# Performance work log

Hardware: AMD Instinct MI355X
Metric: run time of the kernel (lower is better)

Reference implementation:

```python
import jax, jax.numpy as jnp
import numpy as np

# Model dims
B, T, D = 1, 2048, 2048          # batch, seq_len, d_model
HI, DI = 4, 64                   # indexer heads / dim
H, DH = 16, 128                  # attention heads / head dim (H*DH == D)
TOPK = 512                       # sparse top-k tokens per query
NEG = -1e9


def setup_inputs() -> dict:
    key = jax.random.key(0)
    ks = jax.random.split(key, 8)
    s = 0.02  # weight init scale
    return {
        "hidden_states": jax.random.normal(ks[0], (B, T, D), jnp.float32),
        "Wq_idx": jax.random.normal(ks[1], (D, HI * DI), jnp.float32) * s,
        "Wk_idx": jax.random.normal(ks[2], (D, DI), jnp.float32) * s,
        "Ww_idx": jax.random.normal(ks[3], (D, HI), jnp.float32) * s,
        "Wq": jax.random.normal(ks[4], (D, H * DH), jnp.float32) * s,
        "Wk": jax.random.normal(ks[5], (D, H * DH), jnp.float32) * s,
        "Wv": jax.random.normal(ks[6], (D, H * DH), jnp.float32) * s,
        "Wo": jax.random.normal(ks[7], (H * DH, D), jnp.float32) * s,
    }


def reference(hidden_states, Wq_idx, Wk_idx, Ww_idx, Wq, Wk, Wv, Wo):
    x = hidden_states
    # ---- Lightning indexer: I[t,s] = sum_j w[t,j] * relu(q[t,j] . k[s]) ----
    qi = (x @ Wq_idx).reshape(B, T, HI, DI)          # [B,T,HI,DI]
    ki = x @ Wk_idx                                   # [B,S,DI]
    w = x @ Ww_idx                                    # [B,T,HI]
    dots = jnp.einsum('bthd,bsd->bths', qi, ki)       # [B,T,HI,S]
    index_scores = (jax.nn.relu(dots) * w[..., None]).sum(axis=2)  # [B,T,S]

    # ---- Top-k token selection with causal mask ----
    causal = jnp.triu(jnp.ones((T, T), dtype=bool), 1)            # True above diag
    masked_scores = jnp.where(causal[None], NEG, index_scores)
    _, top_idx = jax.lax.top_k(masked_scores, TOPK)               # [B,T,TOPK]
    b_ix = jnp.arange(B)[:, None, None]
    t_ix = jnp.arange(T)[None, :, None]
    top_mask = jnp.zeros((B, T, T), dtype=bool).at[b_ix, t_ix, top_idx].set(True)
    add_mask = jnp.where(top_mask, 0.0, NEG).astype(x.dtype)      # [B,T,S]

    # ---- Dense multi-head attention with additive sparse mask ----
    q = (x @ Wq).reshape(B, T, H, DH)
    k = (x @ Wk).reshape(B, T, H, DH)
    v = (x @ Wv).reshape(B, T, H, DH)
    scores = jnp.einsum('bthd,bshd->bhts', q, k) / np.sqrt(DH).astype(np.float32)
    scores = scores + add_mask[:, None]                            # [B,H,T,S]
    probs = jax.nn.softmax(scores, axis=-1)
    attn = jnp.einsum('bhts,bshd->bthd', probs, v).reshape(B, T, H * DH)
    attn_output = attn @ Wo                                        # [B,T,D]
    return attn_output
```

## Files before the change

kernel.cpp:

```cpp
#include <hip/hip_runtime.h>
#include <cstdint>
#include <cstddef>

#define T_DIM 2048
#define D_DIM 2048
#define HI_N 4
#define DI_N 64
#define H_N 16
#define DH_N 128
#define TOPK_N 512
#define NEG_F (-1e9f)
#define FA_NEG (-1e30f)

typedef __attribute__((ext_vector_type(8))) short short8;
typedef __attribute__((ext_vector_type(4))) float f32x4;
typedef unsigned short ushort_t;

__device__ __forceinline__ unsigned short f2bf(float f) {
  unsigned u = __float_as_uint(f);
  u += 0x7FFFu + ((u >> 16) & 1u);
  return (unsigned short)(u >> 16);
}
__device__ __forceinline__ float bf2f(unsigned short b) {
  return __uint_as_float((unsigned)b << 16);
}

__global__ __launch_bounds__(256) void idx_proj(const float* __restrict__ x,
                                                const float* __restrict__ Wq_idx,
                                                const float* __restrict__ Wk_idx,
                                                const float* __restrict__ Ww_idx,
                                                float* __restrict__ qi,
                                                float* __restrict__ ki,
                                                float* __restrict__ wI) {
  __shared__ float As[2][16][64];
  __shared__ float Bs[2][16][64];
  const int bm = blockIdx.y << 6;
  const int bn_id = blockIdx.x;
  const float* B; float* C; int ldB, cb, ncols;
  if (bn_id < 4)       { B = Wq_idx; C = qi; ldB = 256; cb = bn_id << 6; ncols = 64; }
  else if (bn_id == 4) { B = Wk_idx; C = ki; ldB = 64;  cb = 0;          ncols = 64; }
  else                 { B = Ww_idx; C = wI; ldB = 4;   cb = 0;          ncols = 4;  }
  const int tid = threadIdx.x;
  const int tx = tid & 15, ty = tid >> 4;
  const int am = tid >> 2;
  const int ak = (tid & 3) << 2;
  float acc[4][4] = {};

  float4 a4 = *(const float4*)&x[(size_t)(bm + am) * 2048 + ak];
  float4 b4 = make_float4(0, 0, 0, 0);
  if ((tx << 2) < ncols) b4 = *(const float4*)&B[(size_t)ty * ldB + cb + (tx << 2)];
  As[0][ak + 0][am] = a4.x; As[0][ak + 1][am] = a4.y;
  As[0][ak + 2][am] = a4.z; As[0][ak + 3][am] = a4.w;
  *(float4*)&Bs[0][ty][tx << 2] = b4;

  int p = 0;
  for (int k0 = 0; k0 < 2048; k0 += 16) {
    __syncthreads();
    const bool more = (k0 + 16) < 2048;
    if (more) {
      a4 = *(const float4*)&x[(size_t)(bm + am) * 2048 + k0 + 16 + ak];
      if ((tx << 2) < ncols)
        b4 = *(const float4*)&B[(size_t)(k0 + 16 + ty) * ldB + cb + (tx << 2)];
    }
#pragma unroll
    for (int kk = 0; kk < 16; ++kk) {
      float4 av4 = *(const float4*)&As[p][kk][ty << 2];
      float4 bv4 = *(const float4*)&Bs[p][kk][tx << 2];
      float av[4] = {av4.x, av4.y, av4.z, av4.w};
      float bv[4] = {bv4.x, bv4.y, bv4.z, bv4.w};
#pragma unroll
      for (int i = 0; i < 4; ++i)
#pragma unroll
        for (int j = 0; j < 4; ++j) acc[i][j] += av[i] * bv[j];
    }
    if (more) {
      As[1 - p][ak + 0][am] = a4.x; As[1 - p][ak + 1][am] = a4.y;
      As[1 - p][ak + 2][am] = a4.z; As[1 - p][ak + 3][am] = a4.w;
      *(float4*)&Bs[1 - p][ty][tx << 2] = b4;
    }
    p ^= 1;
  }
#pragma unroll
  for (int i = 0; i < 4; ++i) {
    int m = bm + (ty << 2) + i;
    int n0 = tx << 2;
    if (n0 + 3 < ncols) {
      *(float4*)&C[(size_t)m * ldB + cb + n0] =
          make_float4(acc[i][0], acc[i][1], acc[i][2], acc[i][3]);
    } else {
#pragma unroll
      for (int j = 0; j < 4; ++j)
        if (n0 + j < ncols) C[(size_t)m * ldB + cb + n0 + j] = acc[i][j];
    }
  }
}

__global__ __launch_bounds__(256) void cast_bf16(const float* __restrict__ in,
                                                 ushort_t* __restrict__ out) {
  int i = (blockIdx.x * 256 + threadIdx.x) * 4;
  float4 f = *(const float4*)(in + i);
  ushort4 o;
  o.x = f2bf(f.x); o.y = f2bf(f.y); o.z = f2bf(f.z); o.w = f2bf(f.w);
  *(ushort4*)(out + i) = o;
}

__global__ __launch_bounds__(256) void cast_transpose(const float* __restrict__ in,
                                                      ushort_t* __restrict__ out,
                                                      int R, int C) {
  __shared__ float tile[32][33];
  const int bx = blockIdx.x * 32;
  const int by = blockIdx.y * 32;
  const int tx = threadIdx.x & 31, ty = threadIdx.x >> 5;
#pragma unroll
  for (int i = 0; i < 32; i += 8)
    tile[ty + i][tx] = in[(size_t)(by + ty + i) * C + bx + tx];
  __syncthreads();
#pragma unroll
  for (int i = 0; i < 32; i += 8)
    out[(size_t)(bx + ty + i) * R + by + tx] = f2bf(tile[tx][ty + i]);
}

__global__ __launch_bounds__(256) void transpose_bf(const ushort_t* __restrict__ in,
                                                    ushort_t* __restrict__ out,
                                                    int ldin) {
  __shared__ ushort_t tile[64][68];
  const int bx = blockIdx.x * 64;
  const int by = blockIdx.y * 64;
  const int tid = threadIdx.x;
#pragma unroll
  for (int p = 0; p < 4; ++p) {
    int r = p * 16 + (tid >> 4), c0 = (tid & 15) * 4;
    *(ushort4*)&tile[r][c0] = *(const ushort4*)(in + (size_t)(by + r) * ldin + bx + c0);
  }
  __syncthreads();
#pragma unroll
  for (int p = 0; p < 4; ++p) {
    int r = p * 16 + (tid >> 4), c0 = (tid & 15) * 4;
    ushort4 o;
    o.x = tile[c0 + 0][r]; o.y = tile[c0 + 1][r];
    o.z = tile[c0 + 2][r]; o.w = tile[c0 + 3][r];
    *(ushort4*)(out + (size_t)(bx + r) * T_DIM + by + c0) = o;
  }
}

template <int OUT_BF16>
__global__ __launch_bounds__(256) void gemm_bt(const ushort_t* __restrict__ A,
                                               const ushort_t* __restrict__ Bt,
                                               void* __restrict__ C,
                                               int M, int N, int K) {
  __shared__ __attribute__((aligned(16))) ushort_t As[128 * 64];
  __shared__ __attribute__((aligned(16))) ushort_t Bs[128 * 64];
  const int bm = blockIdx.y << 7;
  const int bn = blockIdx.x << 7;
  const int tid = threadIdx.x;
  const int lane = tid & 63;
  const int wv = tid >> 6;
  const int wm = (wv >> 1) << 6;
  const int wn = (wv & 1) << 6;

  f32x4 acc[4][4] = {};

  const int sr = tid >> 3;
  const int sc = (tid & 7) << 3;
  const ushort_t* ga = A + (size_t)(bm + sr) * K + sc;
  const ushort_t* gb = Bt + (size_t)(bn + sr) * K + sc;
  const size_t rstep = (size_t)32 * K;

  for (int k0 = 0; k0 < K; k0 += 64) {
#pragma unroll
    for (int i = 0; i < 4; ++i) {
      __builtin_amdgcn_global_load_lds(
          (const __attribute__((address_space(1))) unsigned int*)(ga + i * rstep + k0),
          (__attribute__((address_space(3))) unsigned int*)(As + i * 2048 + tid * 8),
          16, 0, 0);
      __builtin_amdgcn_global_load_lds(
          (const __attribute__((address_space(1))) unsigned int*)(gb + i * rstep + k0),
          (__attribute__((address_space(3))) unsigned int*)(Bs + i * 2048 + tid * 8),
          16, 0, 0);
    }
    __syncthreads();
#pragma unroll
    for (int ks = 0; ks < 2; ++ks) {
      short8 af[4], bfr[4];
      const int kk = (ks << 5) + ((lane >> 4) << 3);
#pragma unroll
      for (int i = 0; i < 4; ++i) {
        af[i]  = *(const short8*)(As + (wm + (i << 4) + (lane & 15)) * 64 + kk);
        bfr[i] = *(const short8*)(Bs + (wn + (i << 4) + (lane & 15)) * 64 + kk);
      }
#pragma unroll
      for (int i = 0; i < 4; ++i)
#pragma unroll
        for (int j = 0; j < 4; ++j)
          acc[i][j] = __builtin_amdgcn_mfma_f32_16x16x32_bf16(af[i], bfr[j], acc[i][j], 0, 0, 0);
    }
    __syncthreads();
  }

  const int lrow = (lane >> 4) << 2;
  const int lcol = lane & 15;
#pragma unroll
  for (int i = 0; i < 4; ++i) {
    const int row = bm + wm + (i << 4) + lrow;
#pragma unroll
    for (int j = 0; j < 4; ++j) {
      const int col = bn + wn + (j << 4) + lcol;
#pragma unroll
      for (int r = 0; r < 4; ++r) {
        if (OUT_BF16)
          ((ushort_t*)C)[(size_t)(row + r) * N + col] = f2bf(acc[i][j][r]);
        else
          ((float*)C)[(size_t)(row + r) * N + col] = acc[i][j][r];
      }
    }
  }
}

__global__ __launch_bounds__(256) void idx_scores_rt(const float* __restrict__ qi,
                                                     const float* __restrict__ ki,
                                                     const float* __restrict__ w,
                                                     float* __restrict__ out) {
  const int t0 = blockIdx.y << 6, s0 = blockIdx.x << 6;
  const int tid = threadIdx.x;
  const int tx = tid & 15, ty = tid >> 4;
  if (s0 > t0 + 63) {
    const float4 nf = make_float4(NEG_F, NEG_F, NEG_F, NEG_F);
#pragma unroll
    for (int i = 0; i < 4; ++i) {
      int m = t0 + (ty << 2) + i;
      *(float4*)&out[(size_t)m * T_DIM + s0 + (tx << 2)] = nf;
    }
    return;
  }
  __shared__ float As[16][64];
  __shared__ float Bs[16][64];
  __shared__ float wsh[64][4];
  if (tid < 64) *(float4*)wsh[tid] = *(const float4*)&w[(size_t)(t0 + tid) * 4];
  const int am = tid >> 2;
  const int ak = (tid & 3) << 2;
  float oacc[4][4] = {};
#pragma unroll
  for (int h = 0; h < HI_N; ++h) {
    float dacc[4][4] = {};
    for (int k0 = 0; k0 < DI_N; k0 += 16) {
      float4 qa = *(const float4*)&qi[(size_t)(t0 + am) * 256 + h * DI_N + k0 + ak];
      float4 kb = *(const float4*)&ki[(size_t)(s0 + am) * DI_N + k0 + ak];
      __syncthreads();
      As[ak + 0][am] = qa.x; As[ak + 1][am] = qa.y;
      As[ak + 2][am] = qa.z; As[ak + 3][am] = qa.w;
      Bs[ak + 0][am] = kb.x; Bs[ak + 1][am] = kb.y;
      Bs[ak + 2][am] = kb.z; Bs[ak + 3][am] = kb.w;
      __syncthreads();
#pragma unroll
      for (int kk = 0; kk < 16; ++kk) {
        float4 a4 = *(const float4*)&As[kk][ty << 2];
        float4 b4 = *(const float4*)&Bs[kk][tx << 2];
        float av[4] = {a4.x, a4.y, a4.z, a4.w};
        float bv[4] = {b4.x, b4.y, b4.z, b4.w};
#pragma unroll
        for (int i = 0; i < 4; ++i)
#pragma unroll
          for (int j = 0; j < 4; ++j) dacc[i][j] += av[i] * bv[j];
      }
    }
#pragma unroll
    for (int i = 0; i < 4; ++i) {
      float wh = wsh[(ty << 2) + i][h];
#pragma unroll
      for (int j = 0; j < 4; ++j) oacc[i][j] += fmaxf(dacc[i][j], 0.f) * wh;
    }
  }
#pragma unroll
  for (int i = 0; i < 4; ++i) {
    int m = t0 + (ty << 2) + i;
    int n0 = s0 + (tx << 2);
    float4 r;
    r.x = (n0 + 0 > m) ? NEG_F : oacc[i][0];
    r.y = (n0 + 1 > m) ? NEG_F : oacc[i][1];
    r.z = (n0 + 2 > m) ? NEG_F : oacc[i][2];
    r.w = (n0 + 3 > m) ? NEG_F : oacc[i][3];
    *(float4*)&out[(size_t)m * T_DIM + n0] = r;
  }
}

__global__ __launch_bounds__(256) void select_mask(const float* __restrict__ scores,
                                                   unsigned long long* __restrict__ maskbits) {
  const int t = blockIdx.x, tid = threadIdx.x;
  __shared__ unsigned int hist[256];
  __shared__ unsigned int s_prefix, s_krem;
  __shared__ unsigned char bytes[256];
  unsigned int uv[8];
  const float* row = scores + (size_t)t * T_DIM;
  {
    float4 f0 = *(const float4*)(row + tid * 8);
    float4 f1 = *(const float4*)(row + tid * 8 + 4);
    float fv[8] = {f0.x, f0.y, f0.z, f0.w, f1.x, f1.y, f1.z, f1.w};
#pragma unroll
    for (int j = 0; j < 8; ++j) {
      unsigned u = __float_as_uint(fv[j]);
      uv[j] = (u & 0x80000000u) ? ~u : (u | 0x80000000u);
    }
  }
  if (tid == 0) { s_prefix = 0u; s_krem = TOPK_N; }
  for (int p = 0; p < 4; ++p) {
    const int sh = 24 - 8 * p;
    hist[tid] = 0;
    __syncthreads();
    const unsigned pm = p ? (0xFFFFFFFFu << (32 - 8 * p)) : 0u;
    const unsigned prefix = s_prefix;
#pragma unroll
    for (int j = 0; j < 8; ++j)
      if ((uv[j] & pm) == prefix) atomicAdd(&hist[(uv[j] >> sh) & 255], 1u);
    __syncthreads();
    if (tid == 0) {
      unsigned krem = s_krem, cum = 0;
      int b = 255;
      for (;; --b) { cum += hist[b]; if (cum >= krem) break; }
      s_prefix = prefix | ((unsigned)b << sh);
      s_krem = krem - (cum - hist[b]);
    }
    __syncthreads();
  }
  const unsigned V = s_prefix;
  const int kr = (int)s_krem;
  int eqc = 0;
#pragma unroll
  for (int j = 0; j < 8; ++j) eqc += (uv[j] == V);
  __syncthreads();
  hist[tid] = (unsigned)eqc;
  __syncthreads();
  for (int off = 1; off < 256; off <<= 1) {
    int v = (int)hist[tid];
    if (tid >= off) v += (int)hist[tid - off];
    __syncthreads();
    hist[tid] = (unsigned)v;
    __syncthreads();
  }
  int run = (int)hist[tid] - eqc;
  unsigned char byte = 0;
#pragma unroll
  for (int j = 0; j < 8; ++j) {
    bool eq = (uv[j] == V);
    bool take = (uv[j] > V) || (eq && run < kr);
    run += eq;
    byte |= (unsigned char)(take ? (1u << j) : 0u);
  }
  bytes[tid] = byte;
  __syncthreads();
  if (tid < 32) {
    unsigned long long wqw = 0;
#pragma unroll
    for (int b = 0; b < 8; ++b)
      wqw |= (unsigned long long)bytes[tid * 8 + b] << (8 * b);
    maskbits[(size_t)t * 32 + tid] = wqw;
  }
}

__global__ __launch_bounds__(256, 1) void flash_attn(
    const ushort_t* __restrict__ q, const ushort_t* __restrict__ k,
    const ushort_t* __restrict__ vt, const unsigned long long* __restrict__ maskbits,
    ushort_t* __restrict__ attn, int ldqk) {
  __shared__ __attribute__((aligned(16))) ushort_t Ks[128 * 128];
  __shared__ __attribute__((aligned(16))) ushort_t Vts[128 * 128];
  __shared__ __attribute__((aligned(16))) ushort_t Ps[128 * 136];
  __shared__ float mstate[2][128], lstate[2][128];
  __shared__ float pmax[2][128], psum[2][128];

  const int tt = blockIdx.x;
  const int h  = blockIdx.y;
  const int t0 = tt << 7;
  const int tid = threadIdx.x;
  const int lane = tid & 63;
  const int wv = tid >> 6;
  const int wm = (wv >> 1) << 6;
  const int wn = (wv & 1) << 6;
  const int l15 = lane & 15, l4 = lane >> 4;

  {
    const ushort_t* gq = q + (size_t)(t0 + (tid >> 4)) * ldqk + h * DH_N + (tid & 15) * 8;
#pragma unroll
    for (int p = 0; p < 8; ++p)
      __builtin_amdgcn_global_load_lds(
          (const __attribute__((address_space(1))) unsigned int*)(gq + (size_t)p * 16 * ldqk),
          (__attribute__((address_space(3))) unsigned int*)(Ks + p * 2048 + tid * 8), 16, 0, 0);
  }
  __syncthreads();
  short8 qfrag[4][4];
#pragma unroll
  for (int ks = 0; ks < 4; ++ks)
#pragma unroll
    for (int i = 0; i < 4; ++i)
      qfrag[ks][i] = *(const short8*)(Ks + (wm + i * 16 + l15) * 128 + ks * 32 + l4 * 8);
  if (tid < 128) { mstate[0][tid] = -INFINITY; lstate[0][tid] = 0.f; }

  f32x4 acc[4][4] = {};
  const int nst = (tt < 4) ? 4 : (tt + 1);
  const bool owner = ((wv & 1) == 0) && (l15 == 0);
  const float rsc = 0.08838834764831845f;

  for (int st = 0; st < nst; ++st) {
    const int s0 = st << 7;
    __syncthreads();
    {
      const ushort_t* gk = k + (size_t)(s0 + (tid >> 4)) * ldqk + h * DH_N + (tid & 15) * 8;
      const ushort_t* gv = vt + (size_t)(h * DH_N + (tid >> 4)) * T_DIM + s0 + (tid & 15) * 8;
#pragma unroll
      for (int p = 0; p < 8; ++p) {
        __builtin_amdgcn_global_load_lds(
            (const __attribute__((address_space(1))) unsigned int*)(gk + (size_t)p * 16 * ldqk),
            (__attribute__((address_space(3))) unsigned int*)(Ks + p * 2048 + tid * 8), 16, 0, 0);
        __builtin_amdgcn_global_load_lds(
            (const __attribute__((address_space(1))) unsigned int*)(gv + (size_t)p * 16 * T_DIM),
            (__attribute__((address_space(3))) unsigned int*)(Vts + p * 2048 + tid * 8), 16, 0, 0);
      }
    }
    unsigned long long mw[4][4];
    {
      const int wbase = (s0 >> 6) + (wn >> 6);
#pragma unroll
      for (int i = 0; i < 4; ++i)
#pragma unroll
        for (int r = 0; r < 4; ++r)
          mw[i][r] = maskbits[(size_t)(t0 + wm + i * 16 + l4 * 4 + r) * 32 + wbase];
    }
    __syncthreads();

    f32x4 sacc[4][4] = {};
#pragma unroll
    for (int ks = 0; ks < 4; ++ks) {
      short8 bfr[4];
#pragma unroll
      for (int j = 0; j < 4; ++j)
        bfr[j] = *(const short8*)(Ks + (wn + j * 16 + l15) * 128 + ks * 32 + l4 * 8);
#pragma unroll
      for (int i = 0; i < 4; ++i)
#pragma unroll
        for (int j = 0; j < 4; ++j)
          sacc[i][j] = __builtin_amdgcn_mfma_f32_16x16x32_bf16(qfrag[ks][i], bfr[j], sacc[i][j], 0, 0, 0);
    }
#pragma unroll
    for (int i = 0; i < 4; ++i)
#pragma unroll
      for (int j = 0; j < 4; ++j)
#pragma unroll
        for (int r = 0; r < 4; ++r) {
          bool sel = (mw[i][r] >> (j * 16 + l15)) & 1;
          sacc[i][j][r] = sel ? sacc[i][j][r] * rsc : FA_NEG;
        }
    float pmx[4][4];
#pragma unroll
    for (int i = 0; i < 4; ++i)
#pragma unroll
      for (int r = 0; r < 4; ++r) {
        float m0 = fmaxf(fmaxf(sacc[i][0][r], sacc[i][1][r]), fmaxf(sacc[i][2][r], sacc[i][3][r]));
#pragma unroll
        for (int off = 1; off < 16; off <<= 1) m0 = fmaxf(m0, __shfl_xor(m0, off));
        pmx[i][r] = m0;
      }
    if (l15 == 0)
#pragma unroll
      for (int i = 0; i < 4; ++i)
#pragma unroll
        for (int r = 0; r < 4; ++r)
          pmax[wv & 1][wm + i * 16 + l4 * 4 + r] = pmx[i][r];
    __syncthreads();

    const int rp = st & 1, wp = 1 - rp;
    float nmr[4][4];
#pragma unroll
    for (int i = 0; i < 4; ++i)
#pragma unroll
      for (int r = 0; r < 4; ++r) {
        int rw = wm + i * 16 + l4 * 4 + r;
        nmr[i][r] = fmaxf(mstate[rp][rw], fmaxf(pmax[0][rw], pmax[1][rw]));
      }
    float alpha_c[4];
#pragma unroll
    for (int j = 0; j < 4; ++j) {
      int col = wn + j * 16 + l15;
      float mo = mstate[rp][col];
      float nc = fmaxf(mo, fmaxf(pmax[0][col], pmax[1][col]));
      alpha_c[j] = __expf(mo - nc);
    }
    if (owner)
#pragma unroll
      for (int i = 0; i < 4; ++i)
#pragma unroll
        for (int r = 0; r < 4; ++r)
          mstate[wp][wm + i * 16 + l4 * 4 + r] = nmr[i][r];

    float psr[4][4] = {};
#pragma unroll
    for (int i = 0; i < 4; ++i)
#pragma unroll
      for (int j = 0; j < 4; ++j)
#pragma unroll
        for (int r = 0; r < 4; ++r) {
          float s = sacc[i][j][r];
          float pv = (s <= -1e29f) ? 0.f : __expf(s - nmr[i][r]);
          sacc[i][j][r] = pv;
          psr[i][r] += pv;
        }
#pragma unroll
    for (int i = 0; i < 4; ++i)
#pragma unroll
      for (int j = 0; j < 4; ++j) {
        int col = wn + j * 16 + l15;
#pragma unroll
        for (int r = 0; r < 4; ++r)
          Ps[(wm + i * 16 + l4 * 4 + r) * 136 + col] = f2bf(sacc[i][j][r]);
      }
#pragma unroll
    for (int i = 0; i < 4; ++i)
#pragma unroll
      for (int r = 0; r < 4; ++r) {
        float sv = psr[i][r];
#pragma unroll
        for (int off = 1; off < 16; off <<= 1) sv += __shfl_xor(sv, off);
        psr[i][r] = sv;
      }
    if (l15 == 0)
#pragma unroll
      for (int i = 0; i < 4; ++i)
#pragma unroll
        for (int r = 0; r < 4; ++r)
          psum[wv & 1][wm + i * 16 + l4 * 4 + r] = psr[i][r];
#pragma unroll
    for (int i = 0; i < 4; ++i)
#pragma unroll
      for (int j = 0; j < 4; ++j)
#pragma unroll
        for (int r = 0; r < 4; ++r)
          acc[i][j][r] *= alpha_c[j];
    __syncthreads();

    if (owner)
#pragma unroll
      for (int i = 0; i < 4; ++i)
#pragma unroll
        for (int r = 0; r < 4; ++r) {
          int rw = wm + i * 16 + l4 * 4 + r;
          float al = __expf(mstate[rp][rw] - nmr[i][r]);
          lstate[wp][rw] = al * lstate[rp][rw] + psum[0][rw] + psum[1][rw];
        }
#pragma unroll
    for (int ks = 0; ks < 4; ++ks) {
      short8 af[4], bfr[4];
#pragma unroll
      for (int i = 0; i < 4; ++i)
        af[i] = *(const short8*)(Vts + (wm + i * 16 + l15) * 128 + ks * 32 + l4 * 8);
#pragma unroll
      for (int j = 0; j < 4; ++j)
        bfr[j] = *(const short8*)(Ps + (wn + j * 16 + l15) * 136 + ks * 32 + l4 * 8);
#pragma unroll
      for (int i = 0; i < 4; ++i)
#pragma unroll
        for (int j = 0; j < 4; ++j)
          acc[i][j] = __builtin_amdgcn_mfma_f32_16x16x32_bf16(af[i], bfr[j], acc[i][j], 0, 0, 0);
    }
  }
  __syncthreads();
  const int fp = nst & 1;
  float linv[4];
#pragma unroll
  for (int j = 0; j < 4; ++j) linv[j] = 1.f / lstate[fp][wn + j * 16 + l15];
#pragma unroll
  for (int i = 0; i < 4; ++i)
#pragma unroll
    for (int j = 0; j < 4; ++j) {
      int col = wn + j * 16 + l15;
      int dbase = wm + i * 16 + l4 * 4;
      ushort4 pk;
      pk.x = f2bf(acc[i][j][0] * linv[j]);
      pk.y = f2bf(acc[i][j][1] * linv[j]);
      pk.z = f2bf(acc[i][j][2] * linv[j]);
      pk.w = f2bf(acc[i][j][3] * linv[j]);
      *(ushort4*)(Ps + col * 136 + dbase) = pk;
    }
  __syncthreads();
#pragma unroll
  for (int p = 0; p < 8; ++p) {
    int rw = p * 16 + (tid >> 4);
    int d0 = (tid & 15) * 8;
    *(ulonglong2*)(attn + (size_t)(t0 + rw) * D_DIM + h * DH_N + d0) =
        *(const ulonglong2*)(Ps + rw * 136 + d0);
  }
}

extern "C" void kernel_launch(void* const* d_in, const int* in_sizes, int n_in,
                              void* d_out, int out_size, void* d_ws, size_t ws_size,
                              hipStream_t stream) {
  (void)in_sizes; (void)n_in; (void)out_size; (void)ws_size;
  const float* x      = (const float*)d_in[0];
  const float* Wq_idx = (const float*)d_in[1];
  const float* Wk_idx = (const float*)d_in[2];
  const float* Ww_idx = (const float*)d_in[3];
  const float* Wq     = (const float*)d_in[4];
  const float* Wk     = (const float*)d_in[5];
  const float* Wv     = (const float*)d_in[6];
  const float* Wo     = (const float*)d_in[7];
  float* out = (float*)d_out;

  char* ws = (char*)d_ws;
  const size_t MB = 1ull << 20;
  float*    scores  = (float*)(ws);
  ushort_t* qkv_bf  = (ushort_t*)(ws);
  unsigned long long* maskbits = (unsigned long long*)(ws + 25 * MB + 512 * 1024);
  ushort_t* x_bf    = (ushort_t*)(ws + 26 * MB);
  ushort_t* Wcat_t  = (ushort_t*)(ws + 34 * MB);
  ushort_t* vt_bf   = (ushort_t*)(ws + 34 * MB);
  ushort_t* attn_bf = (ushort_t*)(ws + 42 * MB);
  ushort_t* Wo_t    = (ushort_t*)(ws + 58 * MB);
  float*    qi      = (float*)(ws + 66 * MB);
  float*    ki      = (float*)(ws + 68 * MB);
  float*    wI      = (float*)(ws + 68 * MB + 512 * 1024);

  const dim3 blk(256);
  const dim3 tgrid(D_DIM / 32, D_DIM / 32);

  cast_bf16<<<dim3((D_DIM * T_DIM) / 1024), blk, 0, stream>>>(x, x_bf);
  cast_transpose<<<tgrid, blk, 0, stream>>>(Wq, Wcat_t, D_DIM, D_DIM);
  cast_transpose<<<tgrid, blk, 0, stream>>>(Wk, Wcat_t + (size_t)D_DIM * D_DIM, D_DIM, D_DIM);
  cast_transpose<<<tgrid, blk, 0, stream>>>(Wv, Wcat_t + (size_t)2 * D_DIM * D_DIM, D_DIM, D_DIM);
  cast_transpose<<<tgrid, blk, 0, stream>>>(Wo, Wo_t, D_DIM, D_DIM);

  idx_proj<<<dim3(6, T_DIM / 64), blk, 0, stream>>>(x, Wq_idx, Wk_idx, Ww_idx, qi, ki, wI);
  idx_scores_rt<<<dim3(T_DIM / 64, T_DIM / 64), blk, 0, stream>>>(qi, ki, wI, scores);
  select_mask<<<dim3(T_DIM), blk, 0, stream>>>(scores, maskbits);

  gemm_bt<1><<<dim3(3 * D_DIM / 128, T_DIM / 128), blk, 0, stream>>>(
      x_bf, Wcat_t, qkv_bf, T_DIM, 3 * D_DIM, D_DIM);

  transpose_bf<<<dim3(D_DIM / 64, T_DIM / 64), blk, 0, stream>>>(
      qkv_bf + 2 * D_DIM, vt_bf, 3 * D_DIM);

  flash_attn<<<dim3(T_DIM / 128, H_N), blk, 0, stream>>>(
      qkv_bf, qkv_bf + D_DIM, vt_bf, maskbits, attn_bf, 3 * D_DIM);

  gemm_bt<0><<<dim3(D_DIM / 128, T_DIM / 128), blk, 0, stream>>>(
      attn_bf, Wo_t, out, T_DIM, D_DIM, D_DIM);
}
```

Measured before the change: 597.8 us.

## Double-buffer K tiles with prefetch, XOR-swizzle LDS, and fine-grained waitcnt barriers in flash attention

Makes the K tile double-buffered in shared memory so the next tile's K load is issued during the current iteration. Replaces __syncthreads with explicit vmcnt/lgkmcnt waits plus s_barrier so V loads can still be in flight while QK^T and softmax run. Adds an XOR swizzle to the Q/K/V LDS layout to cut bank conflicts on fragment reads, and raises wave priority around the MFMA loops. This costs an extra 32 KB of LDS, and the hand-counted vmcnt values must exactly match the outstanding loads or the kernel reads stale data.

```diff
diff --git a/kernel.cpp b/kernel.cpp
--- a/kernel.cpp
+++ b/kernel.cpp
@@ -360,7 +360,7 @@
     const ushort_t* __restrict__ q, const ushort_t* __restrict__ k,
     const ushort_t* __restrict__ vt, const unsigned long long* __restrict__ maskbits,
     ushort_t* __restrict__ attn, int ldqk) {
-  __shared__ __attribute__((aligned(16))) ushort_t Ks[128 * 128];
+  __shared__ __attribute__((aligned(16))) ushort_t Ks[2][128 * 128];
   __shared__ __attribute__((aligned(16))) ushort_t Vts[128 * 128];
   __shared__ __attribute__((aligned(16))) ushort_t Ps[128 * 136];
   __shared__ float mstate[2][128], lstate[2][128];
@@ -375,69 +375,105 @@
   const int wm = (wv >> 1) << 6;
   const int wn = (wv & 1) << 6;
   const int l15 = lane & 15, l4 = lane >> 4;
+  const int e3 = l15 & 7;
+  const int scol = (((tid & 15) ^ ((tid >> 4) & 7)) << 3);
+
+  if (tid < 128) { mstate[0][tid] = -INFINITY; lstate[0][tid] = 0.f; }
 
   {
-    const ushort_t* gq = q + (size_t)(t0 + (tid >> 4)) * ldqk + h * DH_N + (tid & 15) * 8;
+    const ushort_t* gq = q + (size_t)(t0 + (tid >> 4)) * ldqk + h * DH_N + scol;
 #pragma unroll
     for (int p = 0; p < 8; ++p)
       __builtin_amdgcn_global_load_lds(
           (const __attribute__((address_space(1))) unsigned int*)(gq + (size_t)p * 16 * ldqk),
-          (__attribute__((address_space(3))) unsigned int*)(Ks + p * 2048 + tid * 8), 16, 0, 0);
-  }
-  __syncthreads();
+          (__attribute__((address_space(3))) unsigned int*)(Ks[0] + p * 2048 + tid * 8), 16, 0, 0);
+  }
+  asm volatile("s_waitcnt vmcnt(0)" ::: "memory");
+  __builtin_amdgcn_s_barrier();
+  asm volatile("" ::: "memory");
   short8 qfrag[4][4];
 #pragma unroll
   for (int ks = 0; ks < 4; ++ks)
 #pragma unroll
     for (int i = 0; i < 4; ++i)
-      qfrag[ks][i] = *(const short8*)(Ks + (wm + i * 16 + l15) * 128 + ks * 32 + l4 * 8);
-  if (tid < 128) { mstate[0][tid] = -INFINITY; lstate[0][tid] = 0.f; }
+      qfrag[ks][i] = *(const short8*)(Ks[0] + (wm + i * 16 + l15) * 128 +
+                                      ((((ks << 2) + l4) ^ e3) << 3));
+  asm volatile("s_waitcnt lgkmcnt(0)" ::: "memory");
+  __builtin_amdgcn_s_barrier();
+  asm volatile("" ::: "memory");
 
   f32x4 acc[4][4] = {};
   const int nst = (tt < 4) ? 4 : (tt + 1);
   const bool owner = ((wv & 1) == 0) && (l15 == 0);
   const float rsc = 0.08838834764831845f;
 
+  {
+    const ushort_t* gk = k + (size_t)(tid >> 4) * ldqk + h * DH_N + scol;
+#pragma unroll
+    for (int p = 0; p < 8; ++p)
+      __builtin_amdgcn_global_load_lds(
+          (const __attribute__((address_space(1))) unsigned int*)(gk + (size_t)p * 16 * ldqk),
+          (__attribute__((address_space(3))) unsigned int*)(Ks[0] + p * 2048 + tid * 8), 16, 0, 0);
+  }
+
   for (int st = 0; st < nst; ++st) {
     const int s0 = st << 7;
-    __syncthreads();
+    const bool pf = (st + 1) < nst;
+
+    asm volatile("" ::: "memory");
+    __builtin_amdgcn_s_barrier();
+    asm volatile("" ::: "memory");
+
+    unsigned long long mw[4][4];
     {
-      const ushort_t* gk = k + (size_t)(s0 + (tid >> 4)) * ldqk + h * DH_N + (tid & 15) * 8;
-      const ushort_t* gv = vt + (size_t)(h * DH_N + (tid >> 4)) * T_DIM + s0 + (tid & 15) * 8;
-#pragma unroll
-      for (int p = 0; p < 8; ++p) {
-        __builtin_amdgcn_global_load_lds(
-            (const __attribute__((address_space(1))) unsigned int*)(gk + (size_t)p * 16 * ldqk),
-            (__attribute__((address_space(3))) unsigned int*)(Ks + p * 2048 + tid * 8), 16, 0, 0);
+      const int wbase = (s0 >> 6) + (wn >> 6);
+#pragma unroll
+      for (int i = 0; i < 4; ++i)
+#pragma unroll
+        for (int r = 0; r < 4; ++r)
+          mw[i][r] = maskbits[(size_t)(t0 + wm + i * 16 + l4 * 4 + r) * 32 + wbase];
+    }
+    {
+      const ushort_t* gv = vt + (size_t)(h * DH_N + (tid >> 4)) * T_DIM + s0 + scol;
+#pragma unroll
+      for (int p = 0; p < 8; ++p)
         __builtin_amdgcn_global_load_lds(
             (const __attribute__((address_space(1))) unsigned int*)(gv + (size_t)p * 16 * T_DIM),
             (__attribute__((address_space(3))) unsigned int*)(Vts + p * 2048 + tid * 8), 16, 0, 0);
-      }
-    }
-    unsigned long long mw[4][4];
-    {
-      const int wbase = (s0 >> 6) + (wn >> 6);
-#pragma unroll
-      for (int i = 0; i < 4; ++i)
-#pragma unroll
-        for (int r = 0; r < 4; ++r)
-          mw[i][r] = maskbits[(size_t)(t0 + wm + i * 16 + l4 * 4 + r) * 32 + wbase];
-    }
-    __syncthreads();
-
+    }
+    asm volatile("" ::: "memory");
+    if (pf) {
+      const ushort_t* gk = k + (size_t)(s0 + 128 + (tid >> 4)) * ldqk + h * DH_N + scol;
+      ushort_t* dst = Ks[(st + 1) & 1];
+#pragma unroll
+      for (int p = 0; p < 8; ++p)
+        __builtin_amdgcn_global_load_lds(
+            (const __attribute__((address_space(1))) unsigned int*)(gk + (size_t)p * 16 * ldqk),
+            (__attribute__((address_space(3))) unsigned int*)(dst + p * 2048 + tid * 8), 16, 0, 0);
+    }
+    if (pf) asm volatile("s_waitcnt vmcnt(32)" ::: "memory");
+    else    asm volatile("s_waitcnt vmcnt(24)" ::: "memory");
+    __builtin_amdgcn_s_barrier();
+    asm volatile("" ::: "memory");
+
+    const ushort_t* Kb = Ks[st & 1];
     f32x4 sacc[4][4] = {};
+    __builtin_amdgcn_s_setprio(1);
 #pragma unroll
     for (int ks = 0; ks < 4; ++ks) {
       short8 bfr[4];
+      const int co = ((((ks << 2) + l4) ^ e3) << 3);
 #pragma unroll
       for (int j = 0; j < 4; ++j)
-        bfr[j] = *(const short8*)(Ks + (wn + j * 16 + l15) * 128 + ks * 32 + l4 * 8);
+        bfr[j] = *(const short8*)(Kb + (wn + j * 16 + l15) * 128 + co);
 #pragma unroll
       for (int i = 0; i < 4; ++i)
 #pragma unroll
         for (int j = 0; j < 4; ++j)
           sacc[i][j] = __builtin_amdgcn_mfma_f32_16x16x32_bf16(qfrag[ks][i], bfr[j], sacc[i][j], 0, 0, 0);
     }
+    __builtin_amdgcn_s_setprio(0);
+
 #pragma unroll
     for (int i = 0; i < 4; ++i)
 #pragma unroll
@@ -463,7 +499,9 @@
 #pragma unroll
         for (int r = 0; r < 4; ++r)
           pmax[wv & 1][wm + i * 16 + l4 * 4 + r] = pmx[i][r];
-    __syncthreads();
+    asm volatile("s_waitcnt lgkmcnt(0)" ::: "memory");
+    __builtin_amdgcn_s_barrier();
+    asm volatile("" ::: "memory");
 
     const int rp = st & 1, wp = 1 - rp;
     float nmr[4][4];
@@ -532,7 +570,12 @@
 #pragma unroll
         for (int r = 0; r < 4; ++r)
           acc[i][j][r] *= alpha_c[j];
-    __syncthreads();
+
+    asm volatile("s_waitcnt lgkmcnt(0)" ::: "memory");
+    if (pf) asm volatile("s_waitcnt vmcnt(8)" ::: "memory");
+    else    asm volatile("s_waitcnt vmcnt(0)" ::: "memory");
+    __builtin_amdgcn_s_barrier();
+    asm volatile("" ::: "memory");
 
     if (owner)
 #pragma unroll
@@ -543,12 +586,14 @@
           float al = __expf(mstate[rp][rw] - nmr[i][r]);
           lstate[wp][rw] = al * lstate[rp][rw] + psum[0][rw] + psum[1][rw];
         }
+    __builtin_amdgcn_s_setprio(1);
 #pragma unroll
     for (int ks = 0; ks < 4; ++ks) {
       short8 af[4], bfr[4];
-#pragma unroll
-      for (int i = 0; i < 4; ++i)
-        af[i] = *(const short8*)(Vts + (wm + i * 16 + l15) * 128 + ks * 32 + l4 * 8);
+      const int co = ((((ks << 2) + l4) ^ e3) << 3);
+#pragma unroll
+      for (int i = 0; i < 4; ++i)
+        af[i] = *(const short8*)(Vts + (wm + i * 16 + l15) * 128 + co);
 #pragma unroll
       for (int j = 0; j < 4; ++j)
         bfr[j] = *(const short8*)(Ps + (wn + j * 16 + l15) * 136 + ks * 32 + l4 * 8);
@@ -558,6 +603,7 @@
         for (int j = 0; j < 4; ++j)
           acc[i][j] = __builtin_amdgcn_mfma_f32_16x16x32_bf16(af[i], bfr[j], acc[i][j], 0, 0, 0);
     }
+    __builtin_amdgcn_s_setprio(0);
   }
   __syncthreads();
   const int fp = nst & 1;
```

Result: no change. 586.2 us (-1.9%).
